# Optimization experiments

Measured on AMD Instinct MI355X. Metric: run time of the kernel, lower is better.

Reference implementation:

```python
import jax, jax.numpy as jnp
import numpy as np

D_STATE = 64
HEADDIM = 64
D_CONV = 4
EPS = 1e-5


def _layernorm(x, w, b):
    m = jnp.mean(x, -1, keepdims=True)
    v = jnp.mean((x - m) ** 2, -1, keepdims=True)
    return (x - m) * jax.lax.rsqrt(v + EPS) * w + b


def _mamba2(x, W_in, conv_w, conv_b, dt_bias, A_log, Dh, rms_w, W_out):
    # Mamba2 (SSD) forward: in_proj -> causal depthwise conv + silu -> selective scan
    # -> gated RMSNorm -> out_proj.  ngroups=1, headdim=64, d_state=64.
    Bb, L, _ = x.shape
    d_inner = rms_w.shape[0]
    H = dt_bias.shape[0]
    P = d_inner // H
    conv_dim = d_inner + 2 * D_STATE
    zxbcdt = x @ W_in                                   # [B,L,2*d_inner+2*N+H]
    z = zxbcdt[..., :d_inner]
    xBC = zxbcdt[..., d_inner:d_inner + conv_dim]
    dt = zxbcdt[..., d_inner + conv_dim:]               # [B,L,H]
    # causal depthwise conv1d (kernel D_CONV) + bias + silu
    xpad = jnp.pad(xBC, ((0, 0), (D_CONV - 1, 0), (0, 0)))
    xBC = sum(conv_w[k] * xpad[:, k:k + L] for k in range(D_CONV)) + conv_b
    xBC = jax.nn.silu(xBC)
    xh = xBC[..., :d_inner].reshape(Bb, L, H, P)        # [B,L,H,P]
    Bm = xBC[..., d_inner:d_inner + D_STATE]            # [B,L,N]
    Cm = xBC[..., d_inner + D_STATE:]                   # [B,L,N]
    dt = jax.nn.softplus(dt + dt_bias)                  # [B,L,H]
    A = -jnp.exp(A_log)                                 # [H]
    da = jnp.exp(dt * A)                                # [B,L,H] discrete decay
    dtx = dt[..., None] * xh                            # [B,L,H,P]

    def step(h, inp):
        da_t, dtx_t, B_t, C_t = inp
        h = da_t[:, :, None, None] * h + jnp.einsum('bhp,bn->bhpn', dtx_t, B_t)
        y_t = jnp.einsum('bhpn,bn->bhp', h, C_t)
        return h, y_t

    h0 = jnp.zeros((Bb, H, P, D_STATE), x.dtype)
    _, y = jax.lax.scan(step, h0, (da.transpose(1, 0, 2), dtx.transpose(1, 0, 2, 3),
                                   Bm.transpose(1, 0, 2), Cm.transpose(1, 0, 2)))
    y = y.transpose(1, 0, 2, 3) + Dh[None, None, :, None] * xh   # skip term
    y = y.reshape(Bb, L, d_inner)
    # gated RMSNorm (norm_before_gate=False): rmsnorm(y * silu(z)) * weight
    y = y * jax.nn.silu(z)
    y = y * jax.lax.rsqrt(jnp.mean(y * y, -1, keepdims=True) + EPS) * rms_w
    return y @ W_out


def _mamba_params(key, d_model, pre):
    d_inner = 2 * d_model
    H = d_inner // HEADDIM
    conv_dim = d_inner + 2 * D_STATE
    d_in = 2 * d_inner + 2 * D_STATE + H
    k = jax.random.split(key, 5)
    return {
        pre + '_W_in': jax.random.normal(k[0], (d_model, d_in), jnp.float32) * (d_model ** -0.5),
        pre + '_conv_w': jax.random.normal(k[1], (D_CONV, conv_dim), jnp.float32) * 0.2,
        pre + '_conv_b': jnp.zeros((conv_dim,), jnp.float32),
        pre + '_dt_bias': jnp.log(jnp.expm1(jax.random.uniform(k[2], (H,), jnp.float32, 0.001, 0.1))),
        pre + '_A_log': jnp.log(jax.random.uniform(k[3], (H,), jnp.float32, 1.0, 16.0)),
        pre + '_D': jnp.ones((H,), jnp.float32),
        pre + '_rms_w': jnp.ones((d_inner,), jnp.float32),
        pre + '_W_out': jax.random.normal(k[4], (d_inner, d_model), jnp.float32) * (d_inner ** -0.5),
    }


def setup_inputs() -> dict:
    key = jax.random.key(0)
    ks = jax.random.split(key, 3)
    B, L, C = 8, 1024, 128
    inp = {'x': jax.random.normal(ks[0], (B, L, C), jnp.float32)}
    inp['ln_spa_w'] = jnp.ones((C,), jnp.float32)
    inp['ln_spa_b'] = jnp.zeros((C,), jnp.float32)
    inp['ln_spe_w'] = jnp.ones((L,), jnp.float32)
    inp['ln_spe_b'] = jnp.zeros((L,), jnp.float32)
    inp.update(_mamba_params(ks[1], C, 'spa'))
    inp.update(_mamba_params(ks[2], L, 'spe'))
    return inp


def reference(x, ln_spa_w, ln_spa_b, ln_spe_w, ln_spe_b,
              spa_W_in, spa_conv_w, spa_conv_b, spa_dt_bias, spa_A_log, spa_D, spa_rms_w, spa_W_out,
              spe_W_in, spe_conv_w, spe_conv_b, spe_dt_bias, spe_A_log, spe_D, spe_rms_w, spe_W_out):
    # SSD_Block.forward (drop_path=0 -> identity)
    x_spa = _layernorm(x, ln_spa_w, ln_spa_b)
    x_spa = _mamba2(x_spa, spa_W_in, spa_conv_w, spa_conv_b, spa_dt_bias,
                    spa_A_log, spa_D, spa_rms_w, spa_W_out) + x
    x_spe = x_spa.transpose(0, 2, 1)                      # [B,C,L]
    x_spe = _layernorm(x_spe, ln_spe_w, ln_spe_b)
    x_spe = _mamba2(x_spe, spe_W_in, spe_conv_w, spe_conv_b, spe_dt_bias,
                    spe_A_log, spe_D, spe_rms_w, spe_W_out)
    return x_spe.transpose(0, 2, 1) + x_spa
```

## Files before the change

### kernel.cpp

```cpp
#include <hip/hip_runtime.h>
#include <hip/hip_bf16.h>

#define EPSV 1e-5f

typedef __attribute__((ext_vector_type(8))) short short8v;
typedef __attribute__((ext_vector_type(4))) float f32x4;

__device__ inline unsigned short f2bf(float f) {
  __hip_bfloat16 h = __float2bfloat16(f);
  return *reinterpret_cast<unsigned short*>(&h);
}

__device__ inline float bf2f(unsigned short u) {
  return __uint_as_float(((unsigned int)u) << 16);
}

__device__ inline float siluf(float x) { return x / (1.f + expf(-x)); }

__device__ inline void gload_lds16(const void* g, void* l) {
  __builtin_amdgcn_global_load_lds(
      (const __attribute__((address_space(1))) void*)g,
      (__attribute__((address_space(3))) void*)l, 16, 0, 0);
}

__device__ inline float block_sum(float v, float* lds) {
  #pragma unroll
  for (int o = 32; o; o >>= 1) v += __shfl_xor(v, o);
  int tid = threadIdx.x;
  if ((tid & 63) == 0) lds[tid >> 6] = v;
  __syncthreads();
  float r = lds[0] + lds[1] + lds[2] + lds[3];
  __syncthreads();
  return r;
}

__device__ inline float wave_prefix_incl(float v, int lane) {
  #pragma unroll
  for (int o = 1; o < 64; o <<= 1) {
    float u = __shfl_up(v, o);
    if (lane >= o) v += u;
  }
  return v;
}

__device__ inline void wtconv_tile(const float* __restrict__ W,
                                   unsigned short* __restrict__ Wt,
                                   int K, int N, int bx, int by) {
  __shared__ float tile[64][65];
  int n0 = bx * 64, k0 = by * 64;
  int tid = threadIdx.x;
  int r = tid >> 4, c4 = (tid & 15) * 4;
  #pragma unroll
  for (int i = 0; i < 4; i++) {
    int kk = r + i * 16;
    float4 v = make_float4(0.f, 0.f, 0.f, 0.f);
    if (n0 + c4 < N) v = *reinterpret_cast<const float4*>(&W[(long)(k0 + kk) * N + n0 + c4]);
    tile[kk][c4] = v.x; tile[kk][c4 + 1] = v.y; tile[kk][c4 + 2] = v.z; tile[kk][c4 + 3] = v.w;
  }
  __syncthreads();
  #pragma unroll
  for (int i = 0; i < 4; i++) {
    int nl = r + i * 16;
    if (n0 + nl < N) {
      ushort4 o;
      o.x = f2bf(tile[c4 + 0][nl]);
      o.y = f2bf(tile[c4 + 1][nl]);
      o.z = f2bf(tile[c4 + 2][nl]);
      o.w = f2bf(tile[c4 + 3][nl]);
      *reinterpret_cast<ushort4*>(&Wt[(long)(n0 + nl) * K + k0 + c4]) = o;
    }
  }
}

__global__ __launch_bounds__(256) void ln_wt_fused(const float* __restrict__ x,
                                                   const float* __restrict__ w,
                                                   const float* __restrict__ bb,
                                                   unsigned short* __restrict__ outA,
                                                   const float* __restrict__ W0,
                                                   unsigned short* __restrict__ T0,
                                                   const float* __restrict__ W1,
                                                   unsigned short* __restrict__ T1,
                                                   const float* __restrict__ W2,
                                                   unsigned short* __restrict__ T2,
                                                   const float* __restrict__ W3,
                                                   unsigned short* __restrict__ T3) {
  int id = blockIdx.x;
  if (id < 4096) {
    int tid = threadIdx.x;
    __shared__ float lds[4];
    long row = (long)id * 2 + (tid >> 7);
    int lane = tid & 127;
    int base = (tid >> 7) << 1;
    float v = x[row * 128 + lane];
    float s = v;
    #pragma unroll
    for (int o = 32; o; o >>= 1) s += __shfl_xor(s, o);
    if ((tid & 63) == 0) lds[tid >> 6] = s;
    __syncthreads();
    float m = (lds[base] + lds[base + 1]) * (1.f / 128.f);
    float d = v - m;
    float q = d * d;
    #pragma unroll
    for (int o = 32; o; o >>= 1) q += __shfl_xor(q, o);
    __syncthreads();
    if ((tid & 63) == 0) lds[tid >> 6] = q;
    __syncthreads();
    float inv = rsqrtf((lds[base] + lds[base + 1]) * (1.f / 128.f) + EPSV);
    outA[row * 128 + lane] = f2bf(d * inv * w[lane] + bb[lane]);
  } else {
    id -= 4096;
    if (id < 22)        { int r = id;        wtconv_tile(W0, T0, 128,  644,  r % 11, r / 11); }
    else if (id < 30)   { int r = id - 22;   wtconv_tile(W1, T1, 256,  128,  r % 2,  r / 2); }
    else if (id < 1102) { int r = id - 30;   wtconv_tile(W2, T2, 1024, 4256, r % 67, r / 67); }
    else                { int r = id - 1102; wtconv_tile(W3, T3, 2048, 1024, r % 16, r / 16); }
  }
}

__global__ __launch_bounds__(256) void spe_normT(const float* __restrict__ xspa,
                                                 const float* __restrict__ part2,
                                                 const float* __restrict__ w,
                                                 const float* __restrict__ bb,
                                                 unsigned short* __restrict__ out) {
  __shared__ float tile[128][65];
  int c0 = blockIdx.x * 64, l0 = blockIdx.y * 128, b = blockIdx.z;
  int tid = threadIdx.x;
  int rr = tid >> 4, c4 = (tid & 15) * 4;
  #pragma unroll
  for (int p = 0; p < 8; p++) {
    int l = rr + p * 16;
    f32x4 v = *reinterpret_cast<const f32x4*>(
        &xspa[((long)b * 1024 + l0 + l) * 128 + c0 + c4]);
    tile[l][c4] = v[0]; tile[l][c4 + 1] = v[1];
    tile[l][c4 + 2] = v[2]; tile[l][c4 + 3] = v[3];
  }
  __syncthreads();
  int ch = tid >> 2, lq = tid & 3;
  int gc = c0 + ch;
  int bx = gc >> 6, cl = gc & 63;
  float ssum = 0.f, qsum = 0.f;
  #pragma unroll
  for (int sub = 0; sub < 16; sub++) {
    int by = b * 16 + sub;
    float2 pq = *reinterpret_cast<const float2*>(&part2[(((by * 2 + bx) * 64) + cl) * 2]);
    ssum += pq.x; qsum += pq.y;
  }
  float mm = ssum * (1.f / 1024.f);
  float rstd = rsqrtf(qsum * (1.f / 1024.f) - mm * mm + EPSV);
  #pragma unroll
  for (int j = 0; j < 8; j++) {
    int qidx = lq + j * 4;
    int l = qidx * 4;
    float4 wv = *reinterpret_cast<const float4*>(&w[l0 + l]);
    float4 bv = *reinterpret_cast<const float4*>(&bb[l0 + l]);
    ushort4 o;
    o.x = f2bf((tile[l + 0][ch] - mm) * rstd * wv.x + bv.x);
    o.y = f2bf((tile[l + 1][ch] - mm) * rstd * wv.y + bv.y);
    o.z = f2bf((tile[l + 2][ch] - mm) * rstd * wv.z + bv.z);
    o.w = f2bf((tile[l + 3][ch] - mm) * rstd * wv.w + bv.w);
    *reinterpret_cast<ushort4*>(&out[((long)b * 128 + c0 + ch) * 1024 + l0 + l]) = o;
  }
}

__global__ __launch_bounds__(256) void gemm128_split(const unsigned short* __restrict__ A,
                                                     const unsigned short* __restrict__ Bt,
                                                     unsigned short* __restrict__ zout,
                                                     unsigned short* __restrict__ o2,
                                                     float* __restrict__ o3,
                                                     int M, int N, int K,
                                                     int c1, int c2) {
  __shared__ unsigned short As[2][128 * 32];
  __shared__ unsigned short Bs[2][128 * 32];
  int tid = threadIdx.x;
  int lane = tid & 63, w = tid >> 6;
  int wr = (w >> 1) * 64, wc = (w & 1) * 64;
  int ln15 = lane & 15, kg = lane >> 4;
  int rowBase = blockIdx.y * 128, colBase = blockIdx.x * 128;
  int srow = w * 32 + (lane >> 2);
  int scol = (lane & 3) * 8;
  f32x4 acc[4][4] = {};
  auto stage = [&](int buf, int k0) {
    gload_lds16(&A[(long)(rowBase + srow) * K + k0 + scol], &As[buf][(w * 32) * 32]);
    gload_lds16(&A[(long)(rowBase + srow + 16) * K + k0 + scol], &As[buf][(w * 32 + 16) * 32]);
    gload_lds16(&Bt[(long)(colBase + srow) * K + k0 + scol], &Bs[buf][(w * 32) * 32]);
    gload_lds16(&Bt[(long)(colBase + srow + 16) * K + k0 + scol], &Bs[buf][(w * 32 + 16) * 32]);
  };
  stage(0, 0);
  __syncthreads();
  int cur = 0;
  for (int k0 = 0; k0 < K; k0 += 32) {
    if (k0 + 32 < K) stage(cur ^ 1, k0 + 32);
    short8v af[4], bfr[4];
    #pragma unroll
    for (int mt = 0; mt < 4; mt++)
      af[mt] = *reinterpret_cast<const short8v*>(&As[cur][(wr + mt * 16 + ln15) * 32 + kg * 8]);
    #pragma unroll
    for (int nt = 0; nt < 4; nt++)
      bfr[nt] = *reinterpret_cast<const short8v*>(&Bs[cur][(wc + nt * 16 + ln15) * 32 + kg * 8]);
    #pragma unroll
    for (int mt = 0; mt < 4; mt++)
      #pragma unroll
      for (int nt = 0; nt < 4; nt++)
        acc[mt][nt] = __builtin_amdgcn_mfma_f32_16x16x32_bf16(af[mt], bfr[nt], acc[mt][nt], 0, 0, 0);
    __syncthreads();
    cur ^= 1;
  }
  #pragma unroll
  for (int mt = 0; mt < 4; mt++)
    #pragma unroll
    for (int nt = 0; nt < 4; nt++)
      #pragma unroll
      for (int q = 0; q < 4; q++) {
        int r = rowBase + wr + mt * 16 + kg * 4 + q;
        int c = colBase + wc + nt * 16 + ln15;
        if (c < N) {
          float v = acc[mt][nt][q];
          if (c < c1) zout[(long)r * c1 + c] = f2bf(v);
          else if (c < c2) o2[(long)r * (c2 - c1) + (c - c1)] = f2bf(v);
          else o3[(long)r * (N - c2) + (c - c2)] = v;
        }
      }
}

__global__ __launch_bounds__(256) void gemm128x64_t(const unsigned short* __restrict__ A,
                                                    const unsigned short* __restrict__ Bt,
                                                    const float* __restrict__ R,
                                                    float* __restrict__ out,
                                                    int M, int N, int K) {
  __shared__ unsigned short As[2][128 * 32];
  __shared__ unsigned short Bs[2][64 * 32];
  int tid = threadIdx.x;
  int lane = tid & 63, w = tid >> 6;
  int wr = w * 32;
  int ln15 = lane & 15, kg = lane >> 4;
  int rowBase = blockIdx.y * 128, colBase = blockIdx.x * 64;
  int arow = w * 32 + (lane >> 2);
  int brow = w * 16 + (lane >> 2);
  int scol = (lane & 3) * 8;
  f32x4 acc[2][4] = {};
  auto stage = [&](int buf, int k0) {
    gload_lds16(&A[(long)(rowBase + arow) * K + k0 + scol], &As[buf][(w * 32) * 32]);
    gload_lds16(&A[(long)(rowBase + arow + 16) * K + k0 + scol], &As[buf][(w * 32 + 16) * 32]);
    gload_lds16(&Bt[(long)(colBase + brow) * K + k0 + scol], &Bs[buf][(w * 16) * 32]);
  };
  stage(0, 0);
  __syncthreads();
  int cur = 0;
  for (int k0 = 0; k0 < K; k0 += 32) {
    if (k0 + 32 < K) stage(cur ^ 1, k0 + 32);
    short8v af[2], bfr[4];
    #pragma unroll
    for (int mt = 0; mt < 2; mt++)
      af[mt] = *reinterpret_cast<const short8v*>(&As[cur][(wr + mt * 16 + ln15) * 32 + kg * 8]);
    #pragma unroll
    for (int nt = 0; nt < 4; nt++)
      bfr[nt] = *reinterpret_cast<const short8v*>(&Bs[cur][(nt * 16 + ln15) * 32 + kg * 8]);
    #pragma unroll
    for (int mt = 0; mt < 2; mt++)
      #pragma unroll
      for (int nt = 0; nt < 4; nt++)
        acc[mt][nt] = __builtin_amdgcn_mfma_f32_16x16x32_bf16(af[mt], bfr[nt], acc[mt][nt], 0, 0, 0);
    __syncthreads();
    cur ^= 1;
  }
  #pragma unroll
  for (int mt = 0; mt < 2; mt++)
    #pragma unroll
    for (int nt = 0; nt < 4; nt++)
      #pragma unroll
      for (int q = 0; q < 4; q++) {
        int r = rowBase + wr + mt * 16 + kg * 4 + q;
        int c = colBase + nt * 16 + ln15;
        int bb = r >> 7, ch = r & 127;
        out[(long)bb * 131072 + (long)c * 128 + ch] =
            acc[mt][nt][q] + R[((long)bb * 1024 + c) * 128 + ch];
      }
}

__global__ __launch_bounds__(256) void gemm_mfma1(const unsigned short* __restrict__ A,
                                                  const unsigned short* __restrict__ Bt,
                                                  const float* __restrict__ R,
                                                  float* __restrict__ out,
                                                  float* __restrict__ part2,
                                                  int M, int N, int K) {
  __shared__ unsigned short As[64 * 40];
  __shared__ unsigned short Bs[64 * 40];
  int tid = threadIdx.x;
  int lane = tid & 63, w = tid >> 6;
  int wr = (w >> 1) * 32, wc = (w & 1) * 32;
  int ln15 = lane & 15, kg = lane >> 4;
  int rowBase = blockIdx.y * 64, colBase = blockIdx.x * 64;
  int sm = tid >> 2, skb = (tid & 3) * 8;
  f32x4 acc[2][2] = {};
  for (int k0 = 0; k0 < K; k0 += 32) {
    {
      short8v av = *reinterpret_cast<const short8v*>(&A[(long)(rowBase + sm) * K + k0 + skb]);
      *reinterpret_cast<short8v*>(&As[sm * 40 + skb]) = av;
      int n = colBase + sm;
      short8v bv = {0, 0, 0, 0, 0, 0, 0, 0};
      if (n < N) bv = *reinterpret_cast<const short8v*>(&Bt[(long)n * K + k0 + skb]);
      *reinterpret_cast<short8v*>(&Bs[sm * 40 + skb]) = bv;
    }
    __syncthreads();
    short8v af[2], bfr[2];
    #pragma unroll
    for (int mt = 0; mt < 2; mt++)
      af[mt] = *reinterpret_cast<const short8v*>(&As[(wr + mt * 16 + ln15) * 40 + kg * 8]);
    #pragma unroll
    for (int nt = 0; nt < 2; nt++)
      bfr[nt] = *reinterpret_cast<const short8v*>(&Bs[(wc + nt * 16 + ln15) * 40 + kg * 8]);
    #pragma unroll
    for (int mt = 0; mt < 2; mt++)
      #pragma unroll
      for (int nt = 0; nt < 2; nt++)
        acc[mt][nt] = __builtin_amdgcn_mfma_f32_16x16x32_bf16(af[mt], bfr[nt], acc[mt][nt], 0, 0, 0);
    __syncthreads();
  }
  float sC[2] = {0.f, 0.f}, qC[2] = {0.f, 0.f};
  #pragma unroll
  for (int mt = 0; mt < 2; mt++)
    #pragma unroll
    for (int nt = 0; nt < 2; nt++)
      #pragma unroll
      for (int q = 0; q < 4; q++) {
        int r = rowBase + wr + mt * 16 + kg * 4 + q;
        int c = colBase + wc + nt * 16 + ln15;
        float v = acc[mt][nt][q] + R[(long)r * N + c];
        out[(long)r * N + c] = v;
        sC[nt] += v;
        qC[nt] += v * v;
      }
  __shared__ float redS[4][32], redQ[4][32];
  #pragma unroll
  for (int nt = 0; nt < 2; nt++) {
    sC[nt] += __shfl_xor(sC[nt], 16);
    sC[nt] += __shfl_xor(sC[nt], 32);
    qC[nt] += __shfl_xor(qC[nt], 16);
    qC[nt] += __shfl_xor(qC[nt], 32);
  }
  if (lane < 16) {
    redS[w][ln15] = sC[0];       redQ[w][ln15] = qC[0];
    redS[w][16 + ln15] = sC[1];  redQ[w][16 + ln15] = qC[1];
  }
  __syncthreads();
  if (tid < 64) {
    int c = tid;
    int grp = c >> 5, lo = c & 31;
    float ss = redS[grp][lo] + redS[grp + 2][lo];
    float qq = redQ[grp][lo] + redQ[grp + 2][lo];
    long slot = ((long)(blockIdx.y * 2 + blockIdx.x) * 64 + c) * 2;
    part2[slot] = ss;
    part2[slot + 1] = qq;
  }
}

__global__ __launch_bounds__(256) void conv_dtda(const unsigned short* __restrict__ zx,
                                                 const float* __restrict__ cw,
                                                 const float* __restrict__ cb,
                                                 unsigned short* __restrict__ cout,
                                                 const float* __restrict__ raw,
                                                 const float* __restrict__ dtbias,
                                                 const float* __restrict__ alog,
                                                 float* __restrict__ dt,
                                                 float* __restrict__ la,
                                                 int Bb, int L, int conv_dim,
                                                 int H, int rowsH, int convBlocks) {
  int tid = threadIdx.x;
  if ((int)blockIdx.x < convBlocks) {
    long idx4 = (long)blockIdx.x * 256 + tid;
    int nch4 = conv_dim >> 2;
    long total4 = (long)Bb * L * nch4;
    if (idx4 >= total4) return;
    int ch = (int)(idx4 % nch4) << 2;
    long rt = idx4 / nch4;
    int t = (int)(rt % L);
    int b = (int)(rt / L);
    f32x4 acc = *reinterpret_cast<const f32x4*>(&cb[ch]);
    #pragma unroll
    for (int k = 0; k < 4; k++) {
      int tt = t + k - 3;
      if (tt >= 0) {
        f32x4 wv = *reinterpret_cast<const f32x4*>(&cw[k * conv_dim + ch]);
        ushort4 zu = *reinterpret_cast<const ushort4*>(
            &zx[((long)b * L + tt) * conv_dim + ch]);
        acc[0] += wv[0] * bf2f(zu.x);
        acc[1] += wv[1] * bf2f(zu.y);
        acc[2] += wv[2] * bf2f(zu.z);
        acc[3] += wv[3] * bf2f(zu.w);
      }
    }
    ushort4 o;
    o.x = f2bf(siluf(acc[0])); o.y = f2bf(siluf(acc[1]));
    o.z = f2bf(siluf(acc[2])); o.w = f2bf(siluf(acc[3]));
    *reinterpret_cast<ushort4*>(&cout[rt * conv_dim + ch]) = o;
  } else {
    int idx = ((int)blockIdx.x - convBlocks) * 256 + tid;
    if (idx >= rowsH) return;
    int h = idx % H;
    float v = raw[idx] + dtbias[h];
    float sp = (v > 20.f) ? v : log1pf(expf(v));
    dt[idx] = sp;
    la[idx] = -expf(alog[h]) * sp;
  }
}

__global__ __launch_bounds__(256) void ssd_local(const unsigned short* __restrict__ xbc,
                                                 const float* __restrict__ dtv,
                                                 const float* __restrict__ la,
                                                 float* __restrict__ Sc,
                                                 float* __restrict__ Aprod,
                                                 int NC, int nc_launch, int H,
                                                 int conv_dim, int d_inner) {
  int blk = blockIdx.x;
  int c = blk % nc_launch, bh = blk / nc_launch;
  int h = bh % H, b = bh / H;
  int tid = threadIdx.x;
  long row0 = ((long)(b * NC + c)) * 64;
  __shared__ unsigned short XpT[64 * 72];
  __shared__ unsigned short BT[64 * 72];
  __shared__ float Ws[64];
  int tq = tid >> 4, cq = (tid & 15) << 2;
  ushort4 xr[4], br[4];
  #pragma unroll
  for (int i = 0; i < 4; i++) {
    int t = tq + i * 16;
    const unsigned short* rp = xbc + (row0 + t) * conv_dim;
    xr[i] = *reinterpret_cast<const ushort4*>(rp + (h << 6) + cq);
    br[i] = *reinterpret_cast<const ushort4*>(rp + d_inner + cq);
  }
  if (tid < 64) {
    long r = (row0 + tid) * H + h;
    float cum = wave_prefix_incl(la[r], tid);
    float cT = __shfl(cum, 63);
    Ws[tid] = expf(cT - cum) * dtv[r];
    if (tid == 63) Aprod[(long)bh * NC + c] = expf(cT);
  }
  __syncthreads();
  #pragma unroll
  for (int i = 0; i < 4; i++) {
    int t = tq + i * 16;
    float wv = Ws[t];
    XpT[(cq + 0) * 72 + t] = f2bf(wv * bf2f(xr[i].x));
    XpT[(cq + 1) * 72 + t] = f2bf(wv * bf2f(xr[i].y));
    XpT[(cq + 2) * 72 + t] = f2bf(wv * bf2f(xr[i].z));
    XpT[(cq + 3) * 72 + t] = f2bf(wv * bf2f(xr[i].w));
    BT[(cq + 0) * 72 + t] = br[i].x;
    BT[(cq + 1) * 72 + t] = br[i].y;
    BT[(cq + 2) * 72 + t] = br[i].z;
    BT[(cq + 3) * 72 + t] = br[i].w;
  }
  __syncthreads();
  int lane = tid & 63, wv2 = tid >> 6;
  int wr = (wv2 >> 1) * 32, wc = (wv2 & 1) * 32;
  int ln15 = lane & 15, kg = lane >> 4;
  f32x4 acc[2][2] = {};
  #pragma unroll
  for (int ks = 0; ks < 2; ks++) {
    short8v af[2], bq[2];
    #pragma unroll
    for (int mt = 0; mt < 2; mt++)
      af[mt] = *reinterpret_cast<const short8v*>(&XpT[(wr + mt * 16 + ln15) * 72 + ks * 32 + kg * 8]);
    #pragma unroll
    for (int nt = 0; nt < 2; nt++)
      bq[nt] = *reinterpret_cast<const short8v*>(&BT[(wc + nt * 16 + ln15) * 72 + ks * 32 + kg * 8]);
    #pragma unroll
    for (int mt = 0; mt < 2; mt++)
      #pragma unroll
      for (int nt = 0; nt < 2; nt++)
        acc[mt][nt] = __builtin_amdgcn_mfma_f32_16x16x32_bf16(af[mt], bq[nt], acc[mt][nt], 0, 0, 0);
  }
  float* base = Sc + ((long)bh * NC + c) * 4096;
  #pragma unroll
  for (int mt = 0; mt < 2; mt++)
    #pragma unroll
    for (int nt = 0; nt < 2; nt++)
      #pragma unroll
      for (int q = 0; q < 4; q++) {
        int p = wr + mt * 16 + kg * 4 + q;
        int n = wc + nt * 16 + ln15;
        base[p * 64 + n] = acc[mt][nt][q];
      }
}

__global__ __launch_bounds__(256) void ssd_out(const unsigned short* __restrict__ xbc,
                                               const float* __restrict__ dtv,
                                               const float* __restrict__ la,
                                               const float* __restrict__ Sc,
                                               const float* __restrict__ Aprod,
                                               const float* __restrict__ Dvec,
                                               unsigned short* __restrict__ y,
                                               int NC, int H, int conv_dim,
                                               int d_inner) {
  int blk = blockIdx.x;
  int c = blk % NC, bh = blk / NC;
  int h = bh % H, b = bh / H;
  int tid = threadIdx.x;
  long row0 = ((long)(b * NC + c)) * 64;
  __shared__ unsigned short Cb[64 * 72];
  __shared__ unsigned short Bb[64 * 72];
  __shared__ unsigned short XT[64 * 72];
  __shared__ unsigned short hb[64 * 72];
  __shared__ float Cum[64], Dt[64];
  int tq = tid >> 4, cq = (tid & 15) << 2;
  #pragma unroll
  for (int i = 0; i < 4; i++) {
    int t = tq + i * 16;
    const unsigned short* rp = xbc + (row0 + t) * conv_dim;
    ushort4 cu = *reinterpret_cast<const ushort4*>(rp + d_inner + 64 + cq);
    ushort4 bu = *reinterpret_cast<const ushort4*>(rp + d_inner + cq);
    ushort4 xu = *reinterpret_cast<const ushort4*>(rp + (h << 6) + cq);
    *reinterpret_cast<ushort4*>(&Cb[t * 72 + cq]) = cu;
    *reinterpret_cast<ushort4*>(&Bb[t * 72 + cq]) = bu;
    XT[(cq + 0) * 72 + t] = xu.x;
    XT[(cq + 1) * 72 + t] = xu.y;
    XT[(cq + 2) * 72 + t] = xu.z;
    XT[(cq + 3) * 72 + t] = xu.w;
  }
  if (c > 0) {
    f32x4 hreg[4] = {};
    const float* ap = Aprod + (long)bh * NC;
    for (int j = 0; j < c; j++) {
      const float* sb = Sc + ((long)bh * NC + j) * 4096;
      float a = ap[j];
      #pragma unroll
      for (int i = 0; i < 4; i++) {
        int p = tq + i * 16;
        f32x4 sv = *reinterpret_cast<const f32x4*>(&sb[p * 64 + cq]);
        hreg[i] = hreg[i] * a + sv;
      }
    }
    #pragma unroll
    for (int i = 0; i < 4; i++) {
      int p = tq + i * 16;
      ushort4 ho;
      ho.x = f2bf(hreg[i][0]); ho.y = f2bf(hreg[i][1]);
      ho.z = f2bf(hreg[i][2]); ho.w = f2bf(hreg[i][3]);
      *reinterpret_cast<ushort4*>(&hb[p * 72 + cq]) = ho;
    }
  }
  if (tid < 64) {
    long r = (row0 + tid) * H + h;
    Cum[tid] = wave_prefix_incl(la[r], tid);
    Dt[tid] = dtv[r];
  }
  __syncthreads();
  int lane = tid & 63, wv2 = tid >> 6;
  int wr = (wv2 >> 1) * 32, wc = (wv2 & 1) * 32;
  int ln15 = lane & 15, kg = lane >> 4;
  f32x4 accA[2][2] = {};
  #pragma unroll
  for (int ks = 0; ks < 2; ks++) {
    short8v af[2], bq[2];
    #pragma unroll
    for (int mt = 0; mt < 2; mt++)
      af[mt] = *reinterpret_cast<const short8v*>(&Cb[(wr + mt * 16 + ln15) * 72 + ks * 32 + kg * 8]);
    #pragma unroll
    for (int nt = 0; nt < 2; nt++)
      bq[nt] = *reinterpret_cast<const short8v*>(&Bb[(wc + nt * 16 + ln15) * 72 + ks * 32 + kg * 8]);
    #pragma unroll
    for (int mt = 0; mt < 2; mt++)
      #pragma unroll
      for (int nt = 0; nt < 2; nt++)
        accA[mt][nt] = __builtin_amdgcn_mfma_f32_16x16x32_bf16(af[mt], bq[nt], accA[mt][nt], 0, 0, 0);
  }
  unsigned short gmb[2][2][4];
  #pragma unroll
  for (int mt = 0; mt < 2; mt++)
    #pragma unroll
    for (int nt = 0; nt < 2; nt++)
      #pragma unroll
      for (int q = 0; q < 4; q++) {
        int t = wr + mt * 16 + kg * 4 + q;
        int s = wc + nt * 16 + ln15;
        float v = (s <= t) ? accA[mt][nt][q] * expf(Cum[t] - Cum[s]) * Dt[s] : 0.f;
        gmb[mt][nt][q] = f2bf(v);
      }
  __syncthreads();
  #pragma unroll
  for (int mt = 0; mt < 2; mt++)
    #pragma unroll
    for (int nt = 0; nt < 2; nt++)
      #pragma unroll
      for (int q = 0; q < 4; q++)
        Bb[(wr + mt * 16 + kg * 4 + q) * 72 + wc + nt * 16 + ln15] = gmb[mt][nt][q];
  __syncthreads();
  f32x4 accY[2][2] = {}, accZ[2][2] = {};
  #pragma unroll
  for (int ks = 0; ks < 2; ks++) {
    short8v af[2], bq[2];
    #pragma unroll
    for (int mt = 0; mt < 2; mt++)
      af[mt] = *reinterpret_cast<const short8v*>(&Bb[(wr + mt * 16 + ln15) * 72 + ks * 32 + kg * 8]);
    #pragma unroll
    for (int nt = 0; nt < 2; nt++)
      bq[nt] = *reinterpret_cast<const short8v*>(&XT[(wc + nt * 16 + ln15) * 72 + ks * 32 + kg * 8]);
    #pragma unroll
    for (int mt = 0; mt < 2; mt++)
      #pragma unroll
      for (int nt = 0; nt < 2; nt++)
        accY[mt][nt] = __builtin_amdgcn_mfma_f32_16x16x32_bf16(af[mt], bq[nt], accY[mt][nt], 0, 0, 0);
  }
  if (c > 0) {
    #pragma unroll
    for (int ks = 0; ks < 2; ks++) {
      short8v af[2], bq[2];
      #pragma unroll
      for (int mt = 0; mt < 2; mt++)
        af[mt] = *reinterpret_cast<const short8v*>(&Cb[(wr + mt * 16 + ln15) * 72 + ks * 32 + kg * 8]);
      #pragma unroll
      for (int nt = 0; nt < 2; nt++)
        bq[nt] = *reinterpret_cast<const short8v*>(&hb[(wc + nt * 16 + ln15) * 72 + ks * 32 + kg * 8]);
      #pragma unroll
      for (int mt = 0; mt < 2; mt++)
        #pragma unroll
        for (int nt = 0; nt < 2; nt++)
          accZ[mt][nt] = __builtin_amdgcn_mfma_f32_16x16x32_bf16(af[mt], bq[nt], accZ[mt][nt], 0, 0, 0);
    }
  }
  float Dv = Dvec[h];
  #pragma unroll
  for (int mt = 0; mt < 2; mt++)
    #pragma unroll
    for (int q = 0; q < 4; q++) {
      int t = wr + mt * 16 + kg * 4 + q;
      float wB = expf(Cum[t]);
      const unsigned short* xp = xbc + (row0 + t) * conv_dim + (h << 6);
      unsigned short* yp = y + (row0 + t) * d_inner + (h << 6);
      #pragma unroll
      for (int nt = 0; nt < 2; nt++) {
        int p = wc + nt * 16 + ln15;
        yp[p] = f2bf(accY[mt][nt][q] + accZ[mt][nt][q] * wB + bf2f(xp[p]) * Dv);
      }
    }
}

template <int CPL>
__global__ __launch_bounds__(256) void gate_rms_bf16(const unsigned short* __restrict__ y,
                                                     const unsigned short* __restrict__ z,
                                                     const float* __restrict__ rmsw,
                                                     unsigned short* __restrict__ ab,
                                                     int d_inner) {
  long row = (long)blockIdx.x * 4 + (threadIdx.x >> 6);
  int lane = threadIdx.x & 63;
  const unsigned short* yr = y + row * d_inner;
  const unsigned short* zr = z + row * d_inner;
  float g[CPL];
  float ss = 0.f;
  #pragma unroll
  for (int j = 0; j < CPL / 4; j++) {
    int c = j * 256 + lane * 4;
    ushort4 yv = *reinterpret_cast<const ushort4*>(&yr[c]);
    ushort4 zv = *reinterpret_cast<const ushort4*>(&zr[c]);
    float g0 = bf2f(yv.x) * siluf(bf2f(zv.x));
    float g1 = bf2f(yv.y) * siluf(bf2f(zv.y));
    float g2 = bf2f(yv.z) * siluf(bf2f(zv.z));
    float g3 = bf2f(yv.w) * siluf(bf2f(zv.w));
    g[j * 4 + 0] = g0; g[j * 4 + 1] = g1; g[j * 4 + 2] = g2; g[j * 4 + 3] = g3;
    ss += g0 * g0 + g1 * g1 + g2 * g2 + g3 * g3;
  }
  #pragma unroll
  for (int o = 32; o; o >>= 1) ss += __shfl_xor(ss, o);
  float inv = rsqrtf(ss / (float)d_inner + EPSV);
  #pragma unroll
  for (int j = 0; j < CPL / 4; j++) {
    int c = j * 256 + lane * 4;
    float4 wv = *reinterpret_cast<const float4*>(&rmsw[c]);
    ushort4 o;
    o.x = f2bf(g[j * 4 + 0] * inv * wv.x);
    o.y = f2bf(g[j * 4 + 1] * inv * wv.y);
    o.z = f2bf(g[j * 4 + 2] * inv * wv.z);
    o.w = f2bf(g[j * 4 + 3] * inv * wv.w);
    *reinterpret_cast<ushort4*>(&ab[row * d_inner + c]) = o;
  }
}

extern "C" void kernel_launch(void* const* d_in, const int* in_sizes, int n_in,
                              void* d_out, int out_size, void* d_ws,
                              size_t ws_size, hipStream_t stream) {
  const float* x        = (const float*)d_in[0];
  const float* ln_spa_w = (const float*)d_in[1];
  const float* ln_spa_b = (const float*)d_in[2];
  const float* ln_spe_w = (const float*)d_in[3];
  const float* ln_spe_b = (const float*)d_in[4];
  const float* spa_W_in   = (const float*)d_in[5];
  const float* spa_conv_w = (const float*)d_in[6];
  const float* spa_conv_b = (const float*)d_in[7];
  const float* spa_dt_b   = (const float*)d_in[8];
  const float* spa_A_log  = (const float*)d_in[9];
  const float* spa_D      = (const float*)d_in[10];
  const float* spa_rms_w  = (const float*)d_in[11];
  const float* spa_W_out  = (const float*)d_in[12];
  const float* spe_W_in   = (const float*)d_in[13];
  const float* spe_conv_w = (const float*)d_in[14];
  const float* spe_conv_b = (const float*)d_in[15];
  const float* spe_dt_b   = (const float*)d_in[16];
  const float* spe_A_log  = (const float*)d_in[17];
  const float* spe_D      = (const float*)d_in[18];
  const float* spe_rms_w  = (const float*)d_in[19];
  const float* spe_W_out  = (const float*)d_in[20];
  float* out = (float*)d_out;

  float* ws = (float*)d_ws;
  float* xspa   = ws;
  unsigned short* z = (unsigned short*)(ws + 1048576);
  unsigned short* xbcraw = (unsigned short*)(ws + 3145728);
  float* Sc     = ws + 3145728;
  float* dtraw  = ws + 6291456;
  unsigned short* cv = (unsigned short*)(ws + 6324224);
  float* dtb    = ws + 9469952;
  float* la     = ws + 9502720;
  unsigned short* yb = (unsigned short*)(ws + 9535488);
  unsigned short* Abf     = (unsigned short*)(ws + 11634688);
  unsigned short* Wt_spai = (unsigned short*)(ws + 12683264);
  unsigned short* Wt_spao = (unsigned short*)(ws + 12724480);
  unsigned short* Wt_spei = (unsigned short*)(ws + 12740864);
  unsigned short* Wt_speo = (unsigned short*)(ws + 14919936);

  hipLaunchKernelGGL(ln_wt_fused, dim3(5710), dim3(256), 0, stream,
                     x, ln_spa_w, ln_spa_b, Abf,
                     spa_W_in, Wt_spai, spa_W_out, Wt_spao,
                     spe_W_in, Wt_spei, spe_W_out, Wt_speo);

  hipLaunchKernelGGL(gemm128_split, dim3(6, 64), dim3(256), 0, stream,
                     Abf, Wt_spai, z, xbcraw, dtraw,
                     8192, 644, 128, 256, 640);
  hipLaunchKernelGGL(conv_dtda, dim3(3200), dim3(256), 0, stream,
                     xbcraw, spa_conv_w, spa_conv_b, cv,
                     dtraw, spa_dt_b, spa_A_log, dtb, la,
                     8, 1024, 384, 4, 32768, 3072);
  hipLaunchKernelGGL(ssd_local, dim3(480), dim3(256), 0, stream,
                     cv, dtb, la, Sc, dtraw, 16, 15, 4, 384, 256);
  hipLaunchKernelGGL(ssd_out, dim3(512), dim3(256), 0, stream,
                     cv, dtb, la, Sc, dtraw, spa_D, yb, 16, 4, 384, 256);
  hipLaunchKernelGGL((gate_rms_bf16<4>), dim3(2048), dim3(256), 0, stream,
                     yb, z, spa_rms_w, Abf, 256);
  hipLaunchKernelGGL(gemm_mfma1, dim3(2, 128), dim3(256), 0, stream,
                     Abf, Wt_spao, x, xspa, dtb, 8192, 128, 256);

  hipLaunchKernelGGL(spe_normT, dim3(2, 8, 8), dim3(256), 0, stream,
                     xspa, dtb, ln_spe_w, ln_spe_b, Abf);
  hipLaunchKernelGGL(gemm128_split, dim3(34, 8), dim3(256), 0, stream,
                     Abf, Wt_spei, z, xbcraw, dtraw,
                     1024, 4256, 1024, 2048, 4224);
  hipLaunchKernelGGL(conv_dtda, dim3(2304), dim3(256), 0, stream,
                     xbcraw, spe_conv_w, spe_conv_b, cv,
                     dtraw, spe_dt_b, spe_A_log, dtb, la,
                     8, 128, 2176, 32, 32768, 2176);
  hipLaunchKernelGGL(ssd_local, dim3(256), dim3(256), 0, stream,
                     cv, dtb, la, Sc, dtraw, 2, 1, 32, 2176, 2048);
  hipLaunchKernelGGL(ssd_out, dim3(512), dim3(256), 0, stream,
                     cv, dtb, la, Sc, dtraw, spe_D, yb, 2, 32, 2176, 2048);
  hipLaunchKernelGGL((gate_rms_bf16<32>), dim3(256), dim3(256), 0, stream,
                     yb, z, spe_rms_w, Abf, 2048);
  hipLaunchKernelGGL(gemm128x64_t, dim3(16, 8), dim3(256), 0, stream,
                     Abf, Wt_speo, xspa, out, 1024, 1024, 2048);
}
```

Baseline: 163.8 us.

## Fuse spectral two-chunk SSD into one kernel and double-buffer gemm_mfma1 loads

Replaces the ssd_local plus ssd_out launch pair for the spectral Mamba (two 64-step chunks per sequence) with a single ssd_spe2 kernel. It computes chunk 0's end state in shared memory and uses it directly for chunk 1, which drops one launch and the global round trip of the chunk state. Separately, gemm_mfma1 now stages tiles with global_load_lds into double-buffered LDS, so the next k-slice loads while the current one computes. The padded LDS stride and the N-bounds guard on B are dropped, which risks bank conflicts and assumes N is a multiple of 64.

```diff
diff --git a/kernel.cpp b/kernel.cpp
--- a/kernel.cpp
+++ b/kernel.cpp
@@ -21,17 +21,6 @@
   __builtin_amdgcn_global_load_lds(
       (const __attribute__((address_space(1))) void*)g,
       (__attribute__((address_space(3))) void*)l, 16, 0, 0);
-}
-
-__device__ inline float block_sum(float v, float* lds) {
-  #pragma unroll
-  for (int o = 32; o; o >>= 1) v += __shfl_xor(v, o);
-  int tid = threadIdx.x;
-  if ((tid & 63) == 0) lds[tid >> 6] = v;
-  __syncthreads();
-  float r = lds[0] + lds[1] + lds[2] + lds[3];
-  __syncthreads();
-  return r;
 }
 
 __device__ inline float wave_prefix_incl(float v, int lane) {
@@ -282,38 +271,39 @@
                                                   float* __restrict__ out,
                                                   float* __restrict__ part2,
                                                   int M, int N, int K) {
-  __shared__ unsigned short As[64 * 40];
-  __shared__ unsigned short Bs[64 * 40];
+  __shared__ unsigned short As[2][64 * 32];
+  __shared__ unsigned short Bs[2][64 * 32];
   int tid = threadIdx.x;
   int lane = tid & 63, w = tid >> 6;
   int wr = (w >> 1) * 32, wc = (w & 1) * 32;
   int ln15 = lane & 15, kg = lane >> 4;
   int rowBase = blockIdx.y * 64, colBase = blockIdx.x * 64;
-  int sm = tid >> 2, skb = (tid & 3) * 8;
+  int srow = w * 16 + (lane >> 2);
+  int scol = (lane & 3) * 8;
   f32x4 acc[2][2] = {};
+  auto stage = [&](int buf, int k0) {
+    gload_lds16(&A[(long)(rowBase + srow) * K + k0 + scol], &As[buf][(w * 16) * 32]);
+    gload_lds16(&Bt[(long)(colBase + srow) * K + k0 + scol], &Bs[buf][(w * 16) * 32]);
+  };
+  stage(0, 0);
+  __syncthreads();
+  int cur = 0;
   for (int k0 = 0; k0 < K; k0 += 32) {
-    {
-      short8v av = *reinterpret_cast<const short8v*>(&A[(long)(rowBase + sm) * K + k0 + skb]);
-      *reinterpret_cast<short8v*>(&As[sm * 40 + skb]) = av;
-      int n = colBase + sm;
-      short8v bv = {0, 0, 0, 0, 0, 0, 0, 0};
-      if (n < N) bv = *reinterpret_cast<const short8v*>(&Bt[(long)n * K + k0 + skb]);
-      *reinterpret_cast<short8v*>(&Bs[sm * 40 + skb]) = bv;
-    }
-    __syncthreads();
+    if (k0 + 32 < K) stage(cur ^ 1, k0 + 32);
     short8v af[2], bfr[2];
     #pragma unroll
     for (int mt = 0; mt < 2; mt++)
-      af[mt] = *reinterpret_cast<const short8v*>(&As[(wr + mt * 16 + ln15) * 40 + kg * 8]);
-    #pragma unroll
-    for (int nt = 0; nt < 2; nt++)
-      bfr[nt] = *reinterpret_cast<const short8v*>(&Bs[(wc + nt * 16 + ln15) * 40 + kg * 8]);
+      af[mt] = *reinterpret_cast<const short8v*>(&As[cur][(wr + mt * 16 + ln15) * 32 + kg * 8]);
+    #pragma unroll
+    for (int nt = 0; nt < 2; nt++)
+      bfr[nt] = *reinterpret_cast<const short8v*>(&Bs[cur][(wc + nt * 16 + ln15) * 32 + kg * 8]);
     #pragma unroll
     for (int mt = 0; mt < 2; mt++)
       #pragma unroll
       for (int nt = 0; nt < 2; nt++)
         acc[mt][nt] = __builtin_amdgcn_mfma_f32_16x16x32_bf16(af[mt], bfr[nt], acc[mt][nt], 0, 0, 0);
     __syncthreads();
+    cur ^= 1;
   }
   float sC[2] = {0.f, 0.f}, qC[2] = {0.f, 0.f};
   #pragma unroll
@@ -629,6 +619,264 @@
       for (int nt = 0; nt < 2; nt++) {
         int p = wc + nt * 16 + ln15;
         yp[p] = f2bf(accY[mt][nt][q] + accZ[mt][nt][q] * wB + bf2f(xp[p]) * Dv);
+      }
+    }
+}
+
+__global__ __launch_bounds__(256) void ssd_spe2(const unsigned short* __restrict__ xbc,
+                                                const float* __restrict__ dtv,
+                                                const float* __restrict__ la,
+                                                const float* __restrict__ Dvec,
+                                                unsigned short* __restrict__ y,
+                                                int H, int conv_dim, int d_inner) {
+  int bh = blockIdx.x;
+  int h = bh % H, b = bh / H;
+  int tid = threadIdx.x;
+  __shared__ unsigned short Cb[64 * 72];
+  __shared__ unsigned short Bb[64 * 72];
+  __shared__ unsigned short XT[64 * 72];
+  __shared__ unsigned short BT2[64 * 72];
+  __shared__ unsigned short WXT[64 * 72];
+  __shared__ unsigned short hb[64 * 72];
+  __shared__ float Cum[64], Dt[64], Wsh[64];
+  int tq = tid >> 4, cq = (tid & 15) << 2;
+  int lane = tid & 63, wv2 = tid >> 6;
+  int wr = (wv2 >> 1) * 32, wc = (wv2 & 1) * 32;
+  int ln15 = lane & 15, kg = lane >> 4;
+  float Dv = Dvec[h];
+
+  long row0 = (long)b * 128;
+  ushort4 cu[4], bu[4], xu[4];
+  #pragma unroll
+  for (int i = 0; i < 4; i++) {
+    int t = tq + i * 16;
+    const unsigned short* rp = xbc + (row0 + t) * conv_dim;
+    cu[i] = *reinterpret_cast<const ushort4*>(rp + d_inner + 64 + cq);
+    bu[i] = *reinterpret_cast<const ushort4*>(rp + d_inner + cq);
+    xu[i] = *reinterpret_cast<const ushort4*>(rp + (h << 6) + cq);
+  }
+  if (tid < 64) {
+    long r = (row0 + tid) * H + h;
+    float cum = wave_prefix_incl(la[r], tid);
+    float cT = __shfl(cum, 63);
+    Cum[tid] = cum;
+    Dt[tid] = dtv[r];
+    Wsh[tid] = expf(cT - cum) * dtv[r];
+  }
+  __syncthreads();
+  #pragma unroll
+  for (int i = 0; i < 4; i++) {
+    int t = tq + i * 16;
+    float wvv = Wsh[t];
+    *reinterpret_cast<ushort4*>(&Cb[t * 72 + cq]) = cu[i];
+    *reinterpret_cast<ushort4*>(&Bb[t * 72 + cq]) = bu[i];
+    XT[(cq + 0) * 72 + t] = xu[i].x;
+    XT[(cq + 1) * 72 + t] = xu[i].y;
+    XT[(cq + 2) * 72 + t] = xu[i].z;
+    XT[(cq + 3) * 72 + t] = xu[i].w;
+    BT2[(cq + 0) * 72 + t] = bu[i].x;
+    BT2[(cq + 1) * 72 + t] = bu[i].y;
+    BT2[(cq + 2) * 72 + t] = bu[i].z;
+    BT2[(cq + 3) * 72 + t] = bu[i].w;
+    WXT[(cq + 0) * 72 + t] = f2bf(wvv * bf2f(xu[i].x));
+    WXT[(cq + 1) * 72 + t] = f2bf(wvv * bf2f(xu[i].y));
+    WXT[(cq + 2) * 72 + t] = f2bf(wvv * bf2f(xu[i].z));
+    WXT[(cq + 3) * 72 + t] = f2bf(wvv * bf2f(xu[i].w));
+  }
+  __syncthreads();
+  f32x4 accS[2][2] = {};
+  #pragma unroll
+  for (int ks = 0; ks < 2; ks++) {
+    short8v af[2], bq[2];
+    #pragma unroll
+    for (int mt = 0; mt < 2; mt++)
+      af[mt] = *reinterpret_cast<const short8v*>(&WXT[(wr + mt * 16 + ln15) * 72 + ks * 32 + kg * 8]);
+    #pragma unroll
+    for (int nt = 0; nt < 2; nt++)
+      bq[nt] = *reinterpret_cast<const short8v*>(&BT2[(wc + nt * 16 + ln15) * 72 + ks * 32 + kg * 8]);
+    #pragma unroll
+    for (int mt = 0; mt < 2; mt++)
+      #pragma unroll
+      for (int nt = 0; nt < 2; nt++)
+        accS[mt][nt] = __builtin_amdgcn_mfma_f32_16x16x32_bf16(af[mt], bq[nt], accS[mt][nt], 0, 0, 0);
+  }
+  f32x4 accA[2][2] = {};
+  #pragma unroll
+  for (int ks = 0; ks < 2; ks++) {
+    short8v af[2], bq[2];
+    #pragma unroll
+    for (int mt = 0; mt < 2; mt++)
+      af[mt] = *reinterpret_cast<const short8v*>(&Cb[(wr + mt * 16 + ln15) * 72 + ks * 32 + kg * 8]);
+    #pragma unroll
+    for (int nt = 0; nt < 2; nt++)
+      bq[nt] = *reinterpret_cast<const short8v*>(&Bb[(wc + nt * 16 + ln15) * 72 + ks * 32 + kg * 8]);
+    #pragma unroll
+    for (int mt = 0; mt < 2; mt++)
+      #pragma unroll
+      for (int nt = 0; nt < 2; nt++)
+        accA[mt][nt] = __builtin_amdgcn_mfma_f32_16x16x32_bf16(af[mt], bq[nt], accA[mt][nt], 0, 0, 0);
+  }
+  unsigned short gmb[2][2][4];
+  #pragma unroll
+  for (int mt = 0; mt < 2; mt++)
+    #pragma unroll
+    for (int nt = 0; nt < 2; nt++)
+      #pragma unroll
+      for (int q = 0; q < 4; q++) {
+        int t = wr + mt * 16 + kg * 4 + q;
+        int s = wc + nt * 16 + ln15;
+        float v = (s <= t) ? accA[mt][nt][q] * expf(Cum[t] - Cum[s]) * Dt[s] : 0.f;
+        gmb[mt][nt][q] = f2bf(v);
+      }
+  __syncthreads();
+  #pragma unroll
+  for (int mt = 0; mt < 2; mt++)
+    #pragma unroll
+    for (int nt = 0; nt < 2; nt++)
+      #pragma unroll
+      for (int q = 0; q < 4; q++) {
+        Bb[(wr + mt * 16 + kg * 4 + q) * 72 + wc + nt * 16 + ln15] = gmb[mt][nt][q];
+        int p = wr + mt * 16 + kg * 4 + q;
+        int n = wc + nt * 16 + ln15;
+        hb[p * 72 + n] = f2bf(accS[mt][nt][q]);
+      }
+  __syncthreads();
+  f32x4 accY[2][2] = {};
+  #pragma unroll
+  for (int ks = 0; ks < 2; ks++) {
+    short8v af[2], bq[2];
+    #pragma unroll
+    for (int mt = 0; mt < 2; mt++)
+      af[mt] = *reinterpret_cast<const short8v*>(&Bb[(wr + mt * 16 + ln15) * 72 + ks * 32 + kg * 8]);
+    #pragma unroll
+    for (int nt = 0; nt < 2; nt++)
+      bq[nt] = *reinterpret_cast<const short8v*>(&XT[(wc + nt * 16 + ln15) * 72 + ks * 32 + kg * 8]);
+    #pragma unroll
+    for (int mt = 0; mt < 2; mt++)
+      #pragma unroll
+      for (int nt = 0; nt < 2; nt++)
+        accY[mt][nt] = __builtin_amdgcn_mfma_f32_16x16x32_bf16(af[mt], bq[nt], accY[mt][nt], 0, 0, 0);
+  }
+  #pragma unroll
+  for (int mt = 0; mt < 2; mt++)
+    #pragma unroll
+    for (int q = 0; q < 4; q++) {
+      int t = wr + mt * 16 + kg * 4 + q;
+      const unsigned short* xp = xbc + (row0 + t) * conv_dim + (h << 6);
+      unsigned short* yp = y + (row0 + t) * d_inner + (h << 6);
+      #pragma unroll
+      for (int nt = 0; nt < 2; nt++) {
+        int p = wc + nt * 16 + ln15;
+        yp[p] = f2bf(accY[mt][nt][q] + bf2f(xp[p]) * Dv);
+      }
+    }
+  __syncthreads();
+
+  long row1 = row0 + 64;
+  #pragma unroll
+  for (int i = 0; i < 4; i++) {
+    int t = tq + i * 16;
+    const unsigned short* rp = xbc + (row1 + t) * conv_dim;
+    cu[i] = *reinterpret_cast<const ushort4*>(rp + d_inner + 64 + cq);
+    bu[i] = *reinterpret_cast<const ushort4*>(rp + d_inner + cq);
+    xu[i] = *reinterpret_cast<const ushort4*>(rp + (h << 6) + cq);
+  }
+  if (tid < 64) {
+    long r = (row1 + tid) * H + h;
+    Cum[tid] = wave_prefix_incl(la[r], tid);
+    Dt[tid] = dtv[r];
+  }
+  __syncthreads();
+  #pragma unroll
+  for (int i = 0; i < 4; i++) {
+    int t = tq + i * 16;
+    *reinterpret_cast<ushort4*>(&Cb[t * 72 + cq]) = cu[i];
+    *reinterpret_cast<ushort4*>(&Bb[t * 72 + cq]) = bu[i];
+    XT[(cq + 0) * 72 + t] = xu[i].x;
+    XT[(cq + 1) * 72 + t] = xu[i].y;
+    XT[(cq + 2) * 72 + t] = xu[i].z;
+    XT[(cq + 3) * 72 + t] = xu[i].w;
+  }
+  __syncthreads();
+  f32x4 accA1[2][2] = {};
+  #pragma unroll
+  for (int ks = 0; ks < 2; ks++) {
+    short8v af[2], bq[2];
+    #pragma unroll
+    for (int mt = 0; mt < 2; mt++)
+      af[mt] = *reinterpret_cast<const short8v*>(&Cb[(wr + mt * 16 + ln15) * 72 + ks * 32 + kg * 8]);
+    #pragma unroll
+    for (int nt = 0; nt < 2; nt++)
+      bq[nt] = *reinterpret_cast<const short8v*>(&Bb[(wc + nt * 16 + ln15) * 72 + ks * 32 + kg * 8]);
+    #pragma unroll
+    for (int mt = 0; mt < 2; mt++)
+      #pragma unroll
+      for (int nt = 0; nt < 2; nt++)
+        accA1[mt][nt] = __builtin_amdgcn_mfma_f32_16x16x32_bf16(af[mt], bq[nt], accA1[mt][nt], 0, 0, 0);
+  }
+  #pragma unroll
+  for (int mt = 0; mt < 2; mt++)
+    #pragma unroll
+    for (int nt = 0; nt < 2; nt++)
+      #pragma unroll
+      for (int q = 0; q < 4; q++) {
+        int t = wr + mt * 16 + kg * 4 + q;
+        int s = wc + nt * 16 + ln15;
+        float v = (s <= t) ? accA1[mt][nt][q] * expf(Cum[t] - Cum[s]) * Dt[s] : 0.f;
+        gmb[mt][nt][q] = f2bf(v);
+      }
+  __syncthreads();
+  #pragma unroll
+  for (int mt = 0; mt < 2; mt++)
+    #pragma unroll
+    for (int nt = 0; nt < 2; nt++)
+      #pragma unroll
+      for (int q = 0; q < 4; q++)
+        Bb[(wr + mt * 16 + kg * 4 + q) * 72 + wc + nt * 16 + ln15] = gmb[mt][nt][q];
+  __syncthreads();
+  f32x4 accY1[2][2] = {}, accZ1[2][2] = {};
+  #pragma unroll
+  for (int ks = 0; ks < 2; ks++) {
+    short8v af[2], bq[2];
+    #pragma unroll
+    for (int mt = 0; mt < 2; mt++)
+      af[mt] = *reinterpret_cast<const short8v*>(&Bb[(wr + mt * 16 + ln15) * 72 + ks * 32 + kg * 8]);
+    #pragma unroll
+    for (int nt = 0; nt < 2; nt++)
+      bq[nt] = *reinterpret_cast<const short8v*>(&XT[(wc + nt * 16 + ln15) * 72 + ks * 32 + kg * 8]);
+    #pragma unroll
+    for (int mt = 0; mt < 2; mt++)
+      #pragma unroll
+      for (int nt = 0; nt < 2; nt++)
+        accY1[mt][nt] = __builtin_amdgcn_mfma_f32_16x16x32_bf16(af[mt], bq[nt], accY1[mt][nt], 0, 0, 0);
+  }
+  #pragma unroll
+  for (int ks = 0; ks < 2; ks++) {
+    short8v af[2], bq[2];
+    #pragma unroll
+    for (int mt = 0; mt < 2; mt++)
+      af[mt] = *reinterpret_cast<const short8v*>(&Cb[(wr + mt * 16 + ln15) * 72 + ks * 32 + kg * 8]);
+    #pragma unroll
+    for (int nt = 0; nt < 2; nt++)
+      bq[nt] = *reinterpret_cast<const short8v*>(&hb[(wc + nt * 16 + ln15) * 72 + ks * 32 + kg * 8]);
+    #pragma unroll
+    for (int mt = 0; mt < 2; mt++)
+      #pragma unroll
+      for (int nt = 0; nt < 2; nt++)
+        accZ1[mt][nt] = __builtin_amdgcn_mfma_f32_16x16x32_bf16(af[mt], bq[nt], accZ1[mt][nt], 0, 0, 0);
+  }
+  #pragma unroll
+  for (int mt = 0; mt < 2; mt++)
+    #pragma unroll
+    for (int q = 0; q < 4; q++) {
+      int t = wr + mt * 16 + kg * 4 + q;
+      float wB = expf(Cum[t]);
+      const unsigned short* xp = xbc + (row1 + t) * conv_dim + (h << 6);
+      unsigned short* yp = y + (row1 + t) * d_inner + (h << 6);
+      #pragma unroll
+      for (int nt = 0; nt < 2; nt++) {
+        int p = wc + nt * 16 + ln15;
+        yp[p] = f2bf(accY1[mt][nt][q] + accZ1[mt][nt][q] * wB + bf2f(xp[p]) * Dv);
       }
     }
 }
@@ -745,10 +993,8 @@
                      xbcraw, spe_conv_w, spe_conv_b, cv,
                      dtraw, spe_dt_b, spe_A_log, dtb, la,
                      8, 128, 2176, 32, 32768, 2176);
-  hipLaunchKernelGGL(ssd_local, dim3(256), dim3(256), 0, stream,
-                     cv, dtb, la, Sc, dtraw, 2, 1, 32, 2176, 2048);
-  hipLaunchKernelGGL(ssd_out, dim3(512), dim3(256), 0, stream,
-                     cv, dtb, la, Sc, dtraw, spe_D, yb, 2, 32, 2176, 2048);
+  hipLaunchKernelGGL(ssd_spe2, dim3(256), dim3(256), 0, stream,
+                     cv, dtb, la, spe_D, yb, 32, 2176, 2048);
   hipLaunchKernelGGL((gate_rms_bf16<32>), dim3(256), dim3(256), 0, stream,
                      yb, z, spe_rms_w, Abf, 2048);
   hipLaunchKernelGGL(gemm128x64_t, dim3(16, 8), dim3(256), 0, stream,
```

Measured after the change: 157.9 us. 1.04x faster.
